# Performance work log

Hardware: AMD Instinct MI355X
Metric: run time of the kernel (lower is better)

Reference implementation:

```python
import jax, jax.numpy as jnp
import numpy as np

SOBEL_X = jnp.array([[-1., 0., 1.], [-2., 0., 2.], [-1., 0., 1.]], dtype=jnp.float32).reshape(1, 1, 3, 3)
SOBEL_Y = jnp.array([[-1., -2., -1.], [0., 0., 0.], [1., 2., 1.]], dtype=jnp.float32).reshape(1, 1, 3, 3)


def _gray(x):
    # x: (B, 3, H, W) -> (B, 1, H, W)
    if x.shape[1] == 3:
        return 0.299 * x[:, 0:1] + 0.587 * x[:, 1:2] + 0.114 * x[:, 2:3]
    return x


def _edges(g):
    # g: (B, 1, H, W); 3x3 Sobel convs with padding 1 (cross-correlation, like torch conv2d)
    dn = ('NCHW', 'OIHW', 'NCHW')
    ex = jax.lax.conv_general_dilated(g, SOBEL_X, (1, 1), ((1, 1), (1, 1)), dimension_numbers=dn)
    ey = jax.lax.conv_general_dilated(g, SOBEL_Y, (1, 1), ((1, 1), (1, 1)), dimension_numbers=dn)
    return jnp.sqrt(ex * ex + ey * ey)


def setup_inputs() -> dict:
    key = jax.random.key(0)
    k1, k2 = jax.random.split(key)
    pred = jax.random.normal(k1, (32, 3, 512, 512), dtype=jnp.float32)
    target = jax.random.normal(k2, (32, 3, 512, 512), dtype=jnp.float32)
    return {"pred": pred, "target": target}


def reference(pred, target):
    pred_edges = _edges(_gray(pred))
    target_edges = _edges(_gray(target))
    return jnp.mean(jnp.abs(pred_edges - target_edges))
```

## Files before the change

### kernel.cpp

```cpp
#include <hip/hip_runtime.h>


#define BATCH 32
#define HH 512
#define WW 512
#define RR 16
#define BANDS 2
#define TILE_H (RR * BANDS)

__global__ void zero_out_kernel(float* out) { out[0] = 0.0f; }

struct GRow { float v[6]; };

__device__ __forceinline__ void zero_row(GRow& g) {
    #pragma unroll
    for (int i = 0; i < 6; ++i) g.v[i] = 0.0f;
}

__device__ __forceinline__ float grayf(float r, float g, float b) {
    return 0.299f * r + 0.587f * g + 0.114f * b;
}

__device__ __forceinline__ void gray_row(
    const float* __restrict__ pbase, const float* __restrict__ tbase,
    int row, int x, bool okL, bool okR, GRow& gp, GRow& gt)
{
    const size_t img = (size_t)HH * WW;
    const float4 z4 = make_float4(0.f, 0.f, 0.f, 0.f);
    const float* pA = pbase + (size_t)row * WW + x;
    const float* tA = tbase + (size_t)row * WW + x;

    float4 prL = okL ? *(const float4*)(pA - 4)           : z4;
    float4 prM =       *(const float4*)(pA);
    float4 prR = okR ? *(const float4*)(pA + 4)           : z4;
    float4 pgL = okL ? *(const float4*)(pA + img - 4)     : z4;
    float4 pgM =       *(const float4*)(pA + img);
    float4 pgR = okR ? *(const float4*)(pA + img + 4)     : z4;
    float4 pbL = okL ? *(const float4*)(pA + 2 * img - 4) : z4;
    float4 pbM =       *(const float4*)(pA + 2 * img);
    float4 pbR = okR ? *(const float4*)(pA + 2 * img + 4) : z4;
    float4 trL = okL ? *(const float4*)(tA - 4)           : z4;
    float4 trM =       *(const float4*)(tA);
    float4 trR = okR ? *(const float4*)(tA + 4)           : z4;
    float4 tgL = okL ? *(const float4*)(tA + img - 4)     : z4;
    float4 tgM =       *(const float4*)(tA + img);
    float4 tgR = okR ? *(const float4*)(tA + img + 4)     : z4;
    float4 tbL = okL ? *(const float4*)(tA + 2 * img - 4) : z4;
    float4 tbM =       *(const float4*)(tA + 2 * img);
    float4 tbR = okR ? *(const float4*)(tA + 2 * img + 4) : z4;

    gp.v[0] = grayf(prL.w, pgL.w, pbL.w);
    gp.v[1] = grayf(prM.x, pgM.x, pbM.x);
    gp.v[2] = grayf(prM.y, pgM.y, pbM.y);
    gp.v[3] = grayf(prM.z, pgM.z, pbM.z);
    gp.v[4] = grayf(prM.w, pgM.w, pbM.w);
    gp.v[5] = grayf(prR.x, pgR.x, pbR.x);

    gt.v[0] = grayf(trL.w, tgL.w, tbL.w);
    gt.v[1] = grayf(trM.x, tgM.x, tbM.x);
    gt.v[2] = grayf(trM.y, tgM.y, tbM.y);
    gt.v[3] = grayf(trM.z, tgM.z, tbM.z);
    gt.v[4] = grayf(trM.w, tgM.w, tbM.w);
    gt.v[5] = grayf(trR.x, tgR.x, tbR.x);
}

__device__ __forceinline__ float sobel4(
    const GRow& pm1, const GRow& pc0, const GRow& pp1,
    const GRow& tm1, const GRow& tc0, const GRow& tp1)
{
    float s = 0.0f;
    #pragma unroll
    for (int i = 0; i < 4; ++i) {
        float ex = (pm1.v[i+2] - pm1.v[i]) + 2.0f * (pc0.v[i+2] - pc0.v[i])
                 + (pp1.v[i+2] - pp1.v[i]);
        float ey = (pp1.v[i] + 2.0f * pp1.v[i+1] + pp1.v[i+2])
                 - (pm1.v[i] + 2.0f * pm1.v[i+1] + pm1.v[i+2]);
        float ep = sqrtf(ex * ex + ey * ey);

        float fx = (tm1.v[i+2] - tm1.v[i]) + 2.0f * (tc0.v[i+2] - tc0.v[i])
                 + (tp1.v[i+2] - tp1.v[i]);
        float fy = (tp1.v[i] + 2.0f * tp1.v[i+1] + tp1.v[i+2])
                 - (tm1.v[i] + 2.0f * tm1.v[i+1] + tm1.v[i+2]);
        float et = sqrtf(fx * fx + fy * fy);

        s += fabsf(ep - et);
    }
    return s;
}

__global__ __launch_bounds__(256, 2) void edge_loss_kernel(
    const float* __restrict__ pred,
    const float* __restrict__ target,
    float* __restrict__ out)
{
    const int t    = threadIdx.x;
    const int tx   = t & 127;
    const int band = t >> 7;
    const int x    = tx * 4;
    const int b      = blockIdx.y;
    const int yStart = blockIdx.x * TILE_H + band * RR;

    const bool okL = (tx > 0);
    const bool okR = (tx < 127);

    const size_t img = (size_t)HH * WW;
    const float* pbase = pred   + (size_t)b * 3 * img;
    const float* tbase = target + (size_t)b * 3 * img;

    GRow pm1, pc0, tm1, tc0;
    if (yStart - 1 >= 0) gray_row(pbase, tbase, yStart - 1, x, okL, okR, pm1, tm1);
    else { zero_row(pm1); zero_row(tm1); }
    gray_row(pbase, tbase, yStart, x, okL, okR, pc0, tc0);

    float acc = 0.0f;
    #pragma unroll
    for (int k = 0; k < RR; ++k) {
        const int rnext = yStart + k + 1;
        GRow pp1, tp1;
        if (rnext < HH) gray_row(pbase, tbase, rnext, x, okL, okR, pp1, tp1);
        else { zero_row(pp1); zero_row(tp1); }

        acc += sobel4(pm1, pc0, pp1, tm1, tc0, tp1);

        pm1 = pc0; pc0 = pp1;
        tm1 = tc0; tc0 = tp1;
    }

    #pragma unroll
    for (int off = 32; off > 0; off >>= 1)
        acc += __shfl_down(acc, off, 64);

    __shared__ float wsum[4];
    if ((t & 63) == 0) wsum[t >> 6] = acc;
    __syncthreads();
    if (t == 0) {
        const float s = wsum[0] + wsum[1] + wsum[2] + wsum[3];
        const float inv_n = 1.0f / ((float)BATCH * HH * WW);
        atomicAdd(out, s * inv_n);
    }
}

extern "C" void kernel_launch(void* const* d_in, const int* in_sizes, int n_in,
                              void* d_out, int out_size, void* d_ws, size_t ws_size,
                              hipStream_t stream) {
    const float* pred   = (const float*)d_in[0];
    const float* target = (const float*)d_in[1];
    float* out = (float*)d_out;

    zero_out_kernel<<<1, 1, 0, stream>>>(out);

    dim3 grid(HH / TILE_H, BATCH);
    edge_loss_kernel<<<grid, 256, 0, stream>>>(pred, target, out);
}
```

Before: 271.7 us.

## Share horizontal halo gray values via wave shuffles instead of redundant float4 loads

Each thread now loads only its own float4 per channel and gets the left and right neighbouring gray values through cross-lane shuffles. Only the edge lanes of each wave fetch their halo with scalar loads. This cuts the per-row vector loads from 18 to 6 per thread. The rows per wave drop from 16 to 8, the block is remapped as 2x2 waves, and the launch-bounds occupancy target rises to 4, which adds more halo-row reloads per tile and more divergent scalar loads at wave edges.

```diff
diff --git a/kernel.cpp b/kernel.cpp
--- a/kernel.cpp
+++ b/kernel.cpp
@@ -4,9 +4,8 @@
 #define BATCH 32
 #define HH 512
 #define WW 512
-#define RR 16
-#define BANDS 2
-#define TILE_H (RR * BANDS)
+#define RR 8
+#define TILE_H (RR * 2)
 
 __global__ void zero_out_kernel(float* out) { out[0] = 0.0f; }
 
@@ -23,45 +22,47 @@
 
 __device__ __forceinline__ void gray_row(
     const float* __restrict__ pbase, const float* __restrict__ tbase,
-    int row, int x, bool okL, bool okR, GRow& gp, GRow& gt)
+    int row, int x, int lane, GRow& gp, GRow& gt)
 {
     const size_t img = (size_t)HH * WW;
-    const float4 z4 = make_float4(0.f, 0.f, 0.f, 0.f);
-    const float* pA = pbase + (size_t)row * WW + x;
-    const float* tA = tbase + (size_t)row * WW + x;
+    const size_t o = (size_t)row * WW + x;
 
-    float4 prL = okL ? *(const float4*)(pA - 4)           : z4;
-    float4 prM =       *(const float4*)(pA);
-    float4 prR = okR ? *(const float4*)(pA + 4)           : z4;
-    float4 pgL = okL ? *(const float4*)(pA + img - 4)     : z4;
-    float4 pgM =       *(const float4*)(pA + img);
-    float4 pgR = okR ? *(const float4*)(pA + img + 4)     : z4;
-    float4 pbL = okL ? *(const float4*)(pA + 2 * img - 4) : z4;
-    float4 pbM =       *(const float4*)(pA + 2 * img);
-    float4 pbR = okR ? *(const float4*)(pA + 2 * img + 4) : z4;
-    float4 trL = okL ? *(const float4*)(tA - 4)           : z4;
-    float4 trM =       *(const float4*)(tA);
-    float4 trR = okR ? *(const float4*)(tA + 4)           : z4;
-    float4 tgL = okL ? *(const float4*)(tA + img - 4)     : z4;
-    float4 tgM =       *(const float4*)(tA + img);
-    float4 tgR = okR ? *(const float4*)(tA + img + 4)     : z4;
-    float4 tbL = okL ? *(const float4*)(tA + 2 * img - 4) : z4;
-    float4 tbM =       *(const float4*)(tA + 2 * img);
-    float4 tbR = okR ? *(const float4*)(tA + 2 * img + 4) : z4;
+    const float4 pr = *(const float4*)(pbase + o);
+    const float4 pg = *(const float4*)(pbase + o + img);
+    const float4 pb = *(const float4*)(pbase + o + 2 * img);
+    const float4 tr = *(const float4*)(tbase + o);
+    const float4 tg = *(const float4*)(tbase + o + img);
+    const float4 tb = *(const float4*)(tbase + o + 2 * img);
 
-    gp.v[0] = grayf(prL.w, pgL.w, pbL.w);
-    gp.v[1] = grayf(prM.x, pgM.x, pbM.x);
-    gp.v[2] = grayf(prM.y, pgM.y, pbM.y);
-    gp.v[3] = grayf(prM.z, pgM.z, pbM.z);
-    gp.v[4] = grayf(prM.w, pgM.w, pbM.w);
-    gp.v[5] = grayf(prR.x, pgR.x, pbR.x);
+    const float p0 = grayf(pr.x, pg.x, pb.x);
+    const float p1 = grayf(pr.y, pg.y, pb.y);
+    const float p2 = grayf(pr.z, pg.z, pb.z);
+    const float p3 = grayf(pr.w, pg.w, pb.w);
+    const float t0 = grayf(tr.x, tg.x, tb.x);
+    const float t1 = grayf(tr.y, tg.y, tb.y);
+    const float t2 = grayf(tr.z, tg.z, tb.z);
+    const float t3 = grayf(tr.w, tg.w, tb.w);
 
-    gt.v[0] = grayf(trL.w, tgL.w, tbL.w);
-    gt.v[1] = grayf(trM.x, tgM.x, tbM.x);
-    gt.v[2] = grayf(trM.y, tgM.y, tbM.y);
-    gt.v[3] = grayf(trM.z, tgM.z, tbM.z);
-    gt.v[4] = grayf(trM.w, tgM.w, tbM.w);
-    gt.v[5] = grayf(trR.x, tgR.x, tbR.x);
+    float pl = __shfl_up(p3, 1, 64);
+    float pR = __shfl_down(p0, 1, 64);
+    float tl = __shfl_up(t3, 1, 64);
+    float tR = __shfl_down(t0, 1, 64);
+
+    if (lane == 0) {
+        if (x > 0) {
+            pl = grayf(pbase[o - 1], pbase[o - 1 + img], pbase[o - 1 + 2 * img]);
+            tl = grayf(tbase[o - 1], tbase[o - 1 + img], tbase[o - 1 + 2 * img]);
+        } else { pl = 0.0f; tl = 0.0f; }
+    }
+    if (lane == 63) {
+        if (x + 4 < WW) {
+            pR = grayf(pbase[o + 4], pbase[o + 4 + img], pbase[o + 4 + 2 * img]);
+            tR = grayf(tbase[o + 4], tbase[o + 4 + img], tbase[o + 4 + 2 * img]);
+        } else { pR = 0.0f; tR = 0.0f; }
+    }
+
+    gp.v[0] = pl; gp.v[1] = p0; gp.v[2] = p1; gp.v[3] = p2; gp.v[4] = p3; gp.v[5] = pR;
+    gt.v[0] = tl; gt.v[1] = t0; gt.v[2] = t1; gt.v[3] = t2; gt.v[4] = t3; gt.v[5] = tR;
 }
 
 __device__ __forceinline__ float sobel4(
@@ -88,36 +89,35 @@
     return s;
 }
 
-__global__ __launch_bounds__(256, 2) void edge_loss_kernel(
+__global__ __launch_bounds__(256, 4) void edge_loss_kernel(
     const float* __restrict__ pred,
     const float* __restrict__ target,
     float* __restrict__ out)
 {
     const int t    = threadIdx.x;
-    const int tx   = t & 127;
-    const int band = t >> 7;
-    const int x    = tx * 4;
+    const int lane = t & 63;
+    const int wave = t >> 6;
+    const int wx   = wave & 1;
+    const int wy   = wave >> 1;
+    const int x    = wx * 256 + lane * 4;
     const int b      = blockIdx.y;
-    const int yStart = blockIdx.x * TILE_H + band * RR;
-
-    const bool okL = (tx > 0);
-    const bool okR = (tx < 127);
+    const int yStart = blockIdx.x * TILE_H + wy * RR;
 
     const size_t img = (size_t)HH * WW;
     const float* pbase = pred   + (size_t)b * 3 * img;
     const float* tbase = target + (size_t)b * 3 * img;
 
     GRow pm1, pc0, tm1, tc0;
-    if (yStart - 1 >= 0) gray_row(pbase, tbase, yStart - 1, x, okL, okR, pm1, tm1);
+    if (yStart - 1 >= 0) gray_row(pbase, tbase, yStart - 1, x, lane, pm1, tm1);
     else { zero_row(pm1); zero_row(tm1); }
-    gray_row(pbase, tbase, yStart, x, okL, okR, pc0, tc0);
+    gray_row(pbase, tbase, yStart, x, lane, pc0, tc0);
 
     float acc = 0.0f;
     #pragma unroll
     for (int k = 0; k < RR; ++k) {
         const int rnext = yStart + k + 1;
         GRow pp1, tp1;
-        if (rnext < HH) gray_row(pbase, tbase, rnext, x, okL, okR, pp1, tp1);
+        if (rnext < HH) gray_row(pbase, tbase, rnext, x, lane, pp1, tp1);
         else { zero_row(pp1); zero_row(tp1); }
 
         acc += sobel4(pm1, pc0, pp1, tm1, tc0, tp1);
@@ -131,7 +131,7 @@
         acc += __shfl_down(acc, off, 64);
 
     __shared__ float wsum[4];
-    if ((t & 63) == 0) wsum[t >> 6] = acc;
+    if (lane == 0) wsum[wave] = acc;
     __syncthreads();
     if (t == 0) {
         const float s = wsum[0] + wsum[1] + wsum[2] + wsum[3];
```

Measured after the change: 264.4 us. 1.03x faster.
